# Performance work log

Hardware: AMD Instinct MI355X
Metric: run time of the kernel (lower is better)

## Reference

```python
import jax, jax.numpy as jnp
import numpy as np

VOCAB = 50257
WORD_DIM = 300
HIDDEN = 256
BATCH = 256   # number of trees
LEAVES = 1024  # leaves per complete binary tree (power of 2)


def setup_inputs() -> dict:
    key = jax.random.key(0)
    k_ids, k_emb, k_w1, k_b1, k_w2, k_b2 = jax.random.split(key, 6)
    word_ids = jax.random.randint(k_ids, (BATCH, LEAVES), 0, VOCAB)
    emb_table = jax.random.normal(k_emb, (VOCAB, WORD_DIM), dtype=jnp.float32) * 0.1
    W1 = jax.random.normal(k_w1, (WORD_DIM, HIDDEN), dtype=jnp.float32) * (1.0 / np.sqrt(WORD_DIM))
    b1 = jax.random.normal(k_b1, (HIDDEN,), dtype=jnp.float32) * 0.01
    W2 = jax.random.normal(k_w2, (2 * HIDDEN, HIDDEN), dtype=jnp.float32) * (1.0 / np.sqrt(2 * HIDDEN))
    b2 = jax.random.normal(k_b2, (HIDDEN,), dtype=jnp.float32) * 0.01
    return {"word_ids": word_ids, "emb_table": emb_table, "W1": W1, "b1": b1, "W2": W2, "b2": b2}


def reference(word_ids, emb_table, W1, b1, W2, b2):
    # Leaves: embedding lookup + word2hidden linear (no nonlinearity, as in source)
    h = jnp.einsum('blw,wh->blh', emb_table[word_ids], W1) + b1  # [B, L, H]
    # Internal nodes: concat(left, right) @ W2 + b2, level by level up the
    # complete binary tree. Loop count = log2(LEAVES), a small static constant.
    while h.shape[1] > 1:
        B, n, H = h.shape
        pairs = h.reshape(B, n // 2, 2 * H)  # concat of sibling states
        h = jnp.einsum('bnk,kh->bnh', pairs, W2) + b2
    return h[:, 0, :]  # root hidden state per tree: [B, H]
```

## Files before the change

### kernel.cpp

```cpp
#include <hip/hip_runtime.h>
#include <hip/hip_bf16.h>
#include <stdint.h>

#define VOCAB 50257
#define WD 300
#define KP1 320
#define MP 50432

using bf16 = __hip_bfloat16;
typedef __attribute__((ext_vector_type(4))) float f32x4;
typedef __attribute__((ext_vector_type(8))) short bf16x8;

__device__ __forceinline__ void async_load16(const void* g, void* l) {
    __builtin_amdgcn_global_load_lds(
        (const __attribute__((address_space(1))) uint32_t*)(uintptr_t)g,
        (__attribute__((address_space(3))) uint32_t*)l, 16, 0, 0);
}

__global__ void prep_w(const float* __restrict__ W1, const float* __restrict__ W2,
                       const float* __restrict__ b2,
                       bf16* __restrict__ w1t, bf16* __restrict__ w2t,
                       bf16* __restrict__ w2b, float* __restrict__ b4,
                       float* __restrict__ zbuf) {
    if (blockIdx.x == 1344) {
        __shared__ float b2s[256];
        int n = threadIdx.x;
        b2s[n] = b2[n];
        zbuf[n] = 0.0f;
        __syncthreads();
        float acc = b2s[n];
        #pragma unroll 8
        for (int k = 0; k < 256; ++k)
            acc += b2s[k] * (W2[k * 256 + n] + W2[(k + 256) * 256 + n]);
        b4[n] = acc;
        return;
    }
    int idx = blockIdx.x * 256 + threadIdx.x;
    if (idx < 256 * KP1) {
        int n = idx / KP1;
        int k = idx - n * KP1;
        w1t[idx] = __float2bfloat16(k < WD ? W1[k * 256 + n] : 0.0f);
    } else if (idx < 256 * KP1 + 131072) {
        int j = idx - 256 * KP1;
        int n = j >> 9, k = j & 511;
        w2t[j] = __float2bfloat16(W2[k * 256 + n]);
    } else {
        int j = idx - 256 * KP1 - 131072;
        w2b[j] = __float2bfloat16(W2[j]);
    }
}

template <int AMODE, bool OUT_F32>
__device__ __forceinline__ void tile_gemm(
    char* smem, const void* Av, const int* ids,
    const bf16* BT, int Bstr, const float* bias,
    void* C, int Cs, int coff, int K, int As, int m0,
    const float* zbuf)
{
    constexpr int ASZ = (AMODE == 2) ? 16384 : 8192;
    constexpr int BSZ = 16384, STAGE = ASZ + BSZ;

    const int t = threadIdx.x, w = t >> 6, lane = t & 63;
    const int rg = w >> 2, cgr = w & 3, mi = lane & 15, q = lane >> 4;
    const bf16* Ab = (const bf16*)Av;

    int4 idq = {0, 0, 0, 0};
    if constexpr (AMODE == 1) idq = ((const int4*)ids)[m0 + (t >> 2)];

    auto stage = [&](int ke, int buf) {
        char* Asm = smem + buf * STAGE;
        char* Bsm = Asm + ASZ;
        if constexpr (AMODE == 2) {
            const float* A32 = (const float*)Av;
            #pragma unroll
            for (int i = 0; i < 2; ++i) {
                int s = i * 512 + t;
                int row = s >> 3;
                int kcd = (s & 7) ^ (row & 7);
                int k = ke + kcd * 4;
                int grow = m0 + row; if (grow >= VOCAB) grow = VOCAB - 1;
                const float* g = (k <= 296) ? (A32 + (size_t)grow * WD + k) : zbuf;
                async_load16(g, Asm + i * 8192 + w * 1024);
            }
        } else {
            int row = t >> 2;
            int kcd = (t & 3) ^ ((row >> 2) & 3);
            const bf16* g;
            if constexpr (AMODE == 1) {
                int sel = ke >> 8;
                int id = (sel & 2) ? ((sel & 1) ? idq.w : idq.z)
                                   : ((sel & 1) ? idq.y : idq.x);
                g = Ab + (size_t)id * 256 + (ke & 255) + kcd * 8;
            } else {
                g = Ab + (size_t)(m0 + row) * As + ke + kcd * 8;
            }
            async_load16(g, Asm + w * 1024);
        }
        #pragma unroll
        for (int i = 0; i < 2; ++i) {
            int s = i * 512 + t;
            int col = s >> 2;
            int kcd = (s & 3) ^ ((col >> 2) & 3);
            async_load16(BT + (size_t)col * Bstr + ke + kcd * 8,
                         Bsm + i * 8192 + w * 1024);
        }
    };

    f32x4 acc[4][4] = {};

    auto compute = [&](int buf) {
        const char* Asm = smem + buf * STAGE;
        const bf16* Bs16 = (const bf16*)(Asm + ASZ);
        bf16x8 af[4], bfr[4];
        if constexpr (AMODE == 2) {
            const float* As32 = (const float*)Asm;
            #pragma unroll
            for (int r = 0; r < 4; ++r) {
                int row = rg * 64 + r * 16 + mi;
                int sl = row * 8 + ((2 * q) ^ (row & 7));
                f32x4 lo = *(const f32x4*)(As32 + sl * 4);
                f32x4 hi = *(const f32x4*)(As32 + (sl ^ 1) * 4);
                union { bf16x8 v; bf16 hh[8]; } u;
                #pragma unroll
                for (int j = 0; j < 4; ++j) u.hh[j] = __float2bfloat16(lo[j]);
                #pragma unroll
                for (int j = 0; j < 4; ++j) u.hh[4 + j] = __float2bfloat16(hi[j]);
                af[r] = u.v;
            }
        } else {
            const bf16* As16 = (const bf16*)Asm;
            #pragma unroll
            for (int r = 0; r < 4; ++r) {
                int row = rg * 64 + r * 16 + mi;
                int slot = row * 4 + (q ^ ((row >> 2) & 3));
                af[r] = *(const bf16x8*)(As16 + slot * 8);
            }
        }
        #pragma unroll
        for (int c = 0; c < 4; ++c) {
            int col = cgr * 64 + c * 16 + mi;
            int slot = col * 4 + (q ^ ((col >> 2) & 3));
            bfr[c] = *(const bf16x8*)(Bs16 + slot * 8);
        }
        #pragma unroll
        for (int r = 0; r < 4; ++r)
            #pragma unroll
            for (int c = 0; c < 4; ++c)
                acc[r][c] = __builtin_amdgcn_mfma_f32_16x16x32_bf16(af[r], bfr[c], acc[r][c], 0, 0, 0);
    };

    const int S = K >> 5;
    if constexpr (AMODE == 2) {
        stage(0, 0);
        for (int k0 = 0; k0 < S; ++k0) {
            if (k0 + 1 < S) {
                stage((k0 + 1) * 32, (k0 + 1) & 1);
                asm volatile("s_waitcnt vmcnt(4)\n\ts_barrier" ::: "memory");
            } else {
                asm volatile("s_waitcnt vmcnt(0)\n\ts_barrier" ::: "memory");
            }
            compute(k0 & 1);
            asm volatile("s_waitcnt lgkmcnt(0)\n\ts_barrier" ::: "memory");
        }
    } else {
        stage(0, 0);
        if (S > 1) stage(32, 1);
        for (int k0 = 0; k0 < S; ++k0) {
            if (k0 + 1 < S)
                asm volatile("s_waitcnt vmcnt(3)\n\ts_barrier" ::: "memory");
            else
                asm volatile("s_waitcnt vmcnt(0)\n\ts_barrier" ::: "memory");
            if (k0 + 2 < S) stage((k0 + 2) * 32, (k0 + 2) % 3);
            compute(k0 % 3);
        }
    }

    #pragma unroll
    for (int r = 0; r < 4; ++r) {
        int rowb = m0 + rg * 64 + r * 16 + q * 4;
        #pragma unroll
        for (int c = 0; c < 4; ++c) {
            int col = cgr * 64 + c * 16 + mi;
            float bv = bias[col];
            #pragma unroll
            for (int i = 0; i < 4; ++i) {
                float v = acc[r][c][i] + bv;
                size_t o = (size_t)(rowb + i) * Cs + coff + col;
                if (OUT_F32) ((float*)C)[o] = v;
                else         ((bf16*)C)[o] = __float2bfloat16(v);
            }
        }
    }
}

__global__ __launch_bounds__(512)
void combo(const float* __restrict__ emb, const bf16* __restrict__ w1t,
           const float* __restrict__ b1, const bf16* __restrict__ w2t,
           const bf16* __restrict__ w2b, bf16* __restrict__ w4t,
           bf16* __restrict__ proj, const float* __restrict__ zbuf) {
    __shared__ char smem[73728];
    int blk = blockIdx.x;
    if (blk < 8) {
        int j = blk >> 1, s = blk & 1;
        tile_gemm<0, false>(smem, w2t + 256 * (j >> 1), nullptr,
                            w2b + 65536 * (j & 1), 256, zbuf,
                            w4t, 1024, 256 * j, 256, 512, s * 128, nullptr);
    } else {
        tile_gemm<2, false>(smem, emb, nullptr, w1t, KP1, b1,
                            proj, 256, 0, KP1, WD, (blk - 8) * 128, zbuf);
    }
}

__global__ __launch_bounds__(512)
void mainK(const bf16* __restrict__ proj, const int* __restrict__ ids,
           const bf16* __restrict__ w4t, const float* __restrict__ b4,
           bf16* __restrict__ h) {
    __shared__ char smem[73728];
    tile_gemm<1, false>(smem, proj, ids, w4t, 1024, b4,
                        h, 256, 0, 1024, 256, blockIdx.x * 128, nullptr);
}

template <bool OUT_F32>
__global__ __launch_bounds__(512)
void tailC(const bf16* __restrict__ in, const bf16* __restrict__ BT,
           const float* __restrict__ bias, void* __restrict__ out, int RT) {
    __shared__ char smem[147456];
    char* Bs  = smem;
    char* As0 = smem + 131072;

    const int t = threadIdx.x, w = t >> 6, lane = t & 63;
    const int rg = w >> 2, cgr = w & 3, mi = lane & 15, q = lane >> 4;
    const int rt = blockIdx.x >> 2, cg = blockIdx.x & 3;
    const int m0 = rt * 128;
    const int c0 = cg * 64;

    #pragma unroll
    for (int i = 0; i < 16; ++i) {
        int s = i * 512 + t;
        int kc = s >> 8;
        int col = (s >> 2) & 63;
        int slot = s & 3;
        int g = slot ^ ((col >> 2) & 3);
        async_load16(BT + (size_t)(c0 + col) * 1024 + kc * 32 + g * 8,
                     Bs + i * 8192 + w * 1024);
    }

    auto stageA = [&](int r, int buf) {
        int row = t >> 2, slot = t & 3;
        int g = slot ^ ((row >> 1) & 3);
        async_load16(in + (size_t)(m0 + row) * 1024 + r * 32 + g * 8,
                     As0 + buf * 8192 + w * 1024);
    };

    f32x4 acc[4] = {};

    auto computeR = [&](int r, int buf) {
        const bf16* As16 = (const bf16*)(As0 + buf * 8192);
        const bf16* Bc   = (const bf16*)(Bs + r * 4096);
        bf16x8 bfr;
        {
            int col = cgr * 16 + mi;
            int slot = q ^ ((col >> 2) & 3);
            bfr = *(const bf16x8*)(Bc + col * 32 + slot * 8);
        }
        #pragma unroll
        for (int ri = 0; ri < 4; ++ri) {
            int row = rg * 64 + ri * 16 + mi;
            int slot = q ^ ((row >> 1) & 3);
            bf16x8 af = *(const bf16x8*)(As16 + row * 32 + slot * 8);
            acc[ri] = __builtin_amdgcn_mfma_f32_16x16x32_bf16(af, bfr, acc[ri], 0, 0, 0);
        }
    };

    stageA(0, 0);
    for (int r = 0; r < 32; ++r) {
        if (r + 1 < 32) {
            stageA(r + 1, (r + 1) & 1);
            asm volatile("s_waitcnt vmcnt(1)\n\ts_barrier" ::: "memory");
        } else {
            asm volatile("s_waitcnt vmcnt(0)\n\ts_barrier" ::: "memory");
        }
        computeR(r, r & 1);
        asm volatile("s_waitcnt lgkmcnt(0)\n\ts_barrier" ::: "memory");
    }

    const int col = c0 + cgr * 16 + mi;
    const float bv = bias[col];
    #pragma unroll
    for (int ri = 0; ri < 4; ++ri) {
        int rowb = m0 + rg * 64 + ri * 16 + q * 4;
        #pragma unroll
        for (int i = 0; i < 4; ++i) {
            float v = acc[ri][i] + bv;
            size_t o = (size_t)(rowb + i) * 256 + col;
            if (OUT_F32) ((float*)out)[o] = v;
            else         ((bf16*)out)[o] = __float2bfloat16(v);
        }
    }
}

extern "C" void kernel_launch(void* const* d_in, const int* in_sizes, int n_in,
                              void* d_out, int out_size, void* d_ws, size_t ws_size,
                              hipStream_t stream) {
    const int*   ids = (const int*)d_in[0];
    const float* emb = (const float*)d_in[1];
    const float* W1  = (const float*)d_in[2];
    const float* b1  = (const float*)d_in[3];
    const float* W2  = (const float*)d_in[4];
    const float* b2  = (const float*)d_in[5];
    (void)in_sizes; (void)n_in; (void)out_size; (void)ws_size;

    char* ws = (char*)d_ws;
    size_t off = 0;
    float* zbuf = (float*)(ws + off); off += 1024;
    float* b4   = (float*)(ws + off); off += 1024;
    bf16* w1t = (bf16*)(ws + off); off += (size_t)256 * KP1 * 2;
    bf16* w2t = (bf16*)(ws + off); off += (size_t)256 * 512 * 2;
    bf16* w2b = (bf16*)(ws + off); off += (size_t)512 * 256 * 2;
    bf16* w4t = (bf16*)(ws + off); off += (size_t)256 * 1024 * 2;
    bf16* proj = (bf16*)(ws + off); off += (size_t)MP * 256 * 2;
    bf16* h  = (bf16*)(ws + off); off += (size_t)65536 * 256 * 2;
    (void)off;

    bf16* t1 = (bf16*)proj;
    bf16* t2 = t1 + (size_t)16384 * 256;
    bf16* t3 = t2 + (size_t)4096 * 256;

    prep_w<<<1345, 256, 0, stream>>>(W1, W2, b2, w1t, w2t, w2b, b4, zbuf);

    combo<<<402, 512, 0, stream>>>(emb, w1t, b1, w2t, w2b, w4t, proj, zbuf);

    mainK<<<512, 512, 0, stream>>>(proj, ids, w4t, b4, h);

    tailC<false><<<512, 512, 0, stream>>>(h,  w4t, b4, t1, 128);
    tailC<false><<<128, 512, 0, stream>>>(t1, w4t, b4, t2, 32);
    tailC<false><<< 32, 512, 0, stream>>>(t2, w4t, b4, t3, 8);
    tailC<true ><<<  8, 512, 0, stream>>>(t3, w4t, b4, d_out, 2);
}
```

Before: 231.7 us.

## Rework tail GEMM kernels to load A directly from global into registers

Replaces the tail-level kernel with a variant that stages only the B matrix in LDS and has each wave read its A rows straight from global memory into registers, dropping the double-buffered A staging and the per-step barriers. Each block now covers 256 rows instead of 128 and each wave computes a 32x64 output tile, so half as many blocks are launched per level. This cuts LDS traffic and synchronisation, but global A loads are no longer prefetched asynchronously and fewer blocks mean less parallelism on the small upper levels.

```diff
diff --git a/kernel.cpp b/kernel.cpp
--- a/kernel.cpp
+++ b/kernel.cpp
@@ -222,16 +222,14 @@
 
 template <bool OUT_F32>
 __global__ __launch_bounds__(512)
-void tailC(const bf16* __restrict__ in, const bf16* __restrict__ BT,
-           const float* __restrict__ bias, void* __restrict__ out, int RT) {
-    __shared__ char smem[147456];
-    char* Bs  = smem;
-    char* As0 = smem + 131072;
+void tailW(const bf16* __restrict__ in, const bf16* __restrict__ BT,
+           const float* __restrict__ bias, void* __restrict__ out) {
+    __shared__ char smem[131072];
 
     const int t = threadIdx.x, w = t >> 6, lane = t & 63;
-    const int rg = w >> 2, cgr = w & 3, mi = lane & 15, q = lane >> 4;
+    const int mi = lane & 15, q = lane >> 4;
     const int rt = blockIdx.x >> 2, cg = blockIdx.x & 3;
-    const int m0 = rt * 128;
+    const int m0 = rt * 256;
     const int c0 = cg * 64;
 
     #pragma unroll
@@ -242,59 +240,44 @@
         int slot = s & 3;
         int g = slot ^ ((col >> 2) & 3);
         async_load16(BT + (size_t)(c0 + col) * 1024 + kc * 32 + g * 8,
-                     Bs + i * 8192 + w * 1024);
-    }
-
-    auto stageA = [&](int r, int buf) {
-        int row = t >> 2, slot = t & 3;
-        int g = slot ^ ((row >> 1) & 3);
-        async_load16(in + (size_t)(m0 + row) * 1024 + r * 32 + g * 8,
-                     As0 + buf * 8192 + w * 1024);
-    };
-
-    f32x4 acc[4] = {};
-
-    auto computeR = [&](int r, int buf) {
-        const bf16* As16 = (const bf16*)(As0 + buf * 8192);
-        const bf16* Bc   = (const bf16*)(Bs + r * 4096);
-        bf16x8 bfr;
-        {
-            int col = cgr * 16 + mi;
+                     smem + i * 8192 + w * 1024);
+    }
+    asm volatile("s_waitcnt vmcnt(0)\n\ts_barrier" ::: "memory");
+
+    const bf16* Bs = (const bf16*)smem;
+    const bf16* Arow0 = in + (size_t)(m0 + w * 32 + mi) * 1024 + q * 8;
+    const bf16* Arow1 = Arow0 + (size_t)16 * 1024;
+
+    f32x4 acc[2][4] = {};
+
+    #pragma unroll 4
+    for (int ks = 0; ks < 32; ++ks) {
+        bf16x8 a0 = *(const bf16x8*)(Arow0 + ks * 32);
+        bf16x8 a1 = *(const bf16x8*)(Arow1 + ks * 32);
+        #pragma unroll
+        for (int c = 0; c < 4; ++c) {
+            int col = c * 16 + mi;
             int slot = q ^ ((col >> 2) & 3);
-            bfr = *(const bf16x8*)(Bc + col * 32 + slot * 8);
-        }
-        #pragma unroll
-        for (int ri = 0; ri < 4; ++ri) {
-            int row = rg * 64 + ri * 16 + mi;
-            int slot = q ^ ((row >> 1) & 3);
-            bf16x8 af = *(const bf16x8*)(As16 + row * 32 + slot * 8);
-            acc[ri] = __builtin_amdgcn_mfma_f32_16x16x32_bf16(af, bfr, acc[ri], 0, 0, 0);
-        }
-    };
-
-    stageA(0, 0);
-    for (int r = 0; r < 32; ++r) {
-        if (r + 1 < 32) {
-            stageA(r + 1, (r + 1) & 1);
-            asm volatile("s_waitcnt vmcnt(1)\n\ts_barrier" ::: "memory");
-        } else {
-            asm volatile("s_waitcnt vmcnt(0)\n\ts_barrier" ::: "memory");
-        }
-        computeR(r, r & 1);
-        asm volatile("s_waitcnt lgkmcnt(0)\n\ts_barrier" ::: "memory");
-    }
-
-    const int col = c0 + cgr * 16 + mi;
-    const float bv = bias[col];
+            bf16x8 bfr = *(const bf16x8*)(Bs + ks * 2048 + col * 32 + slot * 8);
+            acc[0][c] = __builtin_amdgcn_mfma_f32_16x16x32_bf16(a0, bfr, acc[0][c], 0, 0, 0);
+            acc[1][c] = __builtin_amdgcn_mfma_f32_16x16x32_bf16(a1, bfr, acc[1][c], 0, 0, 0);
+        }
+    }
+
     #pragma unroll
-    for (int ri = 0; ri < 4; ++ri) {
-        int rowb = m0 + rg * 64 + ri * 16 + q * 4;
-        #pragma unroll
-        for (int i = 0; i < 4; ++i) {
-            float v = acc[ri][i] + bv;
-            size_t o = (size_t)(rowb + i) * 256 + col;
-            if (OUT_F32) ((float*)out)[o] = v;
-            else         ((bf16*)out)[o] = __float2bfloat16(v);
+    for (int f = 0; f < 2; ++f) {
+        int rowb = m0 + w * 32 + f * 16 + q * 4;
+        #pragma unroll
+        for (int c = 0; c < 4; ++c) {
+            int col = c0 + c * 16 + mi;
+            float bv = bias[col];
+            #pragma unroll
+            for (int i = 0; i < 4; ++i) {
+                float v = acc[f][c][i] + bv;
+                size_t o = (size_t)(rowb + i) * 256 + col;
+                if (OUT_F32) ((float*)out)[o] = v;
+                else         ((bf16*)out)[o] = __float2bfloat16(v);
+            }
         }
     }
 }
@@ -332,8 +315,8 @@
 
     mainK<<<512, 512, 0, stream>>>(proj, ids, w4t, b4, h);
 
-    tailC<false><<<512, 512, 0, stream>>>(h,  w4t, b4, t1, 128);
-    tailC<false><<<128, 512, 0, stream>>>(t1, w4t, b4, t2, 32);
-    tailC<false><<< 32, 512, 0, stream>>>(t2, w4t, b4, t3, 8);
-    tailC<true ><<<  8, 512, 0, stream>>>(t3, w4t, b4, d_out, 2);
-}
+    tailW<false><<<256, 512, 0, stream>>>(h,  w4t, b4, t1);
+    tailW<false><<< 64, 512, 0, stream>>>(t1, w4t, b4, t2);
+    tailW<false><<< 16, 512, 0, stream>>>(t2, w4t, b4, t3);
+    tailW<true ><<<  4, 512, 0, stream>>>(t3, w4t, b4, d_out);
+}
```

After: 252.9 us. +9.1%, slower.
